# Kernel optimization log

Measured on AMD Instinct MI355X. Metric: run time of the kernel, lower is better.

The kernel has to match this reference:

```python
import jax, jax.numpy as jnp
import numpy as np

INPUTDIM = 256
OUTDIM = 64
GRIDSIZE = 300
BATCH = 2048


def setup_inputs() -> dict:
    key = jax.random.key(0)
    kx, kw = jax.random.split(key)
    x = jax.random.normal(kx, (BATCH, INPUTDIM), dtype=jnp.float32)
    stddev = 1.0 / (np.sqrt(INPUTDIM) * np.sqrt(GRIDSIZE))
    fouriercoeffs = jax.random.normal(kw, (2, OUTDIM, INPUTDIM, GRIDSIZE), dtype=jnp.float32) * stddev
    return {"x": x, "fouriercoeffs": fouriercoeffs}


def reference(x, fouriercoeffs):
    # k: frequencies 1..gridsize, shape [gridsize]
    gridsize = fouriercoeffs.shape[-1]
    k = jnp.arange(1, gridsize + 1, dtype=x.dtype)
    # phase [batch, inputdim, gridsize]
    phase = x[:, :, None] * k[None, None, :]
    c = jnp.cos(phase)
    s = jnp.sin(phase)
    # y[b,j] = sum_{i,k} c[b,i,k]*Wc[j,i,k] + s[b,i,k]*Ws[j,i,k]
    y = jnp.einsum('bik,jik->bj', c, fouriercoeffs[0]) + jnp.einsum('bik,jik->bj', s, fouriercoeffs[1])
    return y
```

## Files before the change

kernel.cpp:

```cpp
#include <hip/hip_runtime.h>
#include <hip/hip_bf16.h>

#define BATCH 2048
#define IDIM  256
#define ODIM  64
#define GRIDN 300

typedef __bf16 bf16x8 __attribute__((ext_vector_type(8)));
typedef float  f32x16 __attribute__((ext_vector_type(16)));
typedef float  f32x2  __attribute__((ext_vector_type(2)));
typedef unsigned int uint4v __attribute__((ext_vector_type(4)));

#define AS1 __attribute__((address_space(1)))
#define AS3 __attribute__((address_space(3)))

__device__ __forceinline__ unsigned short f2bf(float f) {
    return __builtin_bit_cast(unsigned short, __float2bfloat16(f));
}

__global__ __launch_bounds__(256) void fkan_prep(const float* __restrict__ fc,
                                                 char* __restrict__ wp) {
    __shared__ alignas(16) char lds[32768];
    const int blk = blockIdx.x;
    const int ib  = blk & 15;
    const int gb  = blk >> 4;
    const int g0  = gb * 8;
    const int G   = (gb == 37) ? 4 : 8;
    const int q   = threadIdx.x >> 6;
    const int j   = threadIdx.x & 63;

    float vals[2][4][8];
    #pragma unroll
    for (int t = 0; t < 2; ++t) {
        #pragma unroll
        for (int e = 0; e < 4; ++e) {
            const float* src = fc + (((size_t)t * ODIM + j) * IDIM
                                     + (ib * 16 + q * 4 + e)) * GRIDN + g0;
            float4 lo = *(const float4*)(src);
            vals[t][e][0] = lo.x; vals[t][e][1] = lo.y;
            vals[t][e][2] = lo.z; vals[t][e][3] = lo.w;
            if (G == 8) {
                float4 hi = *(const float4*)(src + 4);
                vals[t][e][4] = hi.x; vals[t][e][5] = hi.y;
                vals[t][e][6] = hi.z; vals[t][e][7] = hi.w;
            }
        }
    }
    #pragma unroll
    for (int g = 0; g < 8; ++g) {
        if (g < 4 || G == 8) {
            uint4v dw;
            #pragma unroll
            for (int e = 0; e < 4; ++e)
                dw[e] = (unsigned)f2bf(vals[0][e][g]) | ((unsigned)f2bf(vals[1][e][g]) << 16);
            *(uint4v*)(lds + g * 4096 + q * 1024 + j * 16) = dw;
        }
    }
    __syncthreads();
    char* dst = wp + ((size_t)ib * GRIDN + g0) * 4096;
    for (int w = threadIdx.x * 16; w < G * 4096; w += 256 * 16)
        *(uint4v*)(dst + w) = *(const uint4v*)(lds + w);
}

__global__ __launch_bounds__(256, 4) void fkan_main(const float* __restrict__ x,
                                                    const char* __restrict__ wp,
                                                    float* __restrict__ out) {
    __shared__ alignas(16) char lds[2][12288];

    const int bid    = blockIdx.x;
    const int xcd    = bid & 7;
    const int within = bid >> 3;
    const int slice  = xcd * 8 + (within & 7);
    const int mtile  = within >> 3;
    const int isplit = slice >> 2;
    const int gq     = slice & 3;
    const int g_begin = gq * 75;

    const int tid  = threadIdx.x;
    const int wave = tid >> 6;
    const int lane = tid & 63;
    const int l31  = lane & 31;
    const int kgrp = lane >> 5;
    const int row  = mtile * 128 + wave * 32 + l31;

    f32x2 vc[4], vs[4], vbc[4], vbs[4];
    const float* xrow = x + (size_t)row * IDIM + isplit * 16;
    #pragma unroll
    for (int h = 0; h < 2; ++h) {
        const float4 xv4 = *(const float4*)(xrow + h * 8 + kgrp * 4);
        float xa[4] = {xv4.x, xv4.y, xv4.z, xv4.w};
        #pragma unroll
        for (int p = 0; p < 4; ++p) {
            const int ss = h * 4 + p;
            const float xv = xa[p];
            float sb, cb;
            __sincosf(xv, &sb, &cb);
            vbc[ss >> 1][ss & 1] = cb; vbs[ss >> 1][ss & 1] = sb;
            float s0 = sb, c0 = cb;
            if (g_begin != 0) __sincosf((float)(g_begin + 1) * xv, &s0, &c0);
            vc[ss >> 1][ss & 1] = c0; vs[ss >> 1][ss & 1] = s0;
        }
    }

    const unsigned aq = (unsigned)kgrp * 1024 + (unsigned)l31 * 16;
    const char* wbase = wp + ((size_t)(isplit * GRIDN + g_begin)) * 4096 + tid * 16;

    #pragma unroll
    for (int p = 0; p < 3; ++p)
        __builtin_amdgcn_global_load_lds(
            (const AS1 unsigned int*)(wbase + (size_t)p * 4096),
            (AS3 unsigned int*)(&lds[0][0] + p * 4096 + tid * 16), 16, 0, 0);
    __syncthreads();

    f32x16 acc0 = {0,0,0,0,0,0,0,0,0,0,0,0,0,0,0,0};
    f32x16 acc1 = {0,0,0,0,0,0,0,0,0,0,0,0,0,0,0,0};

    for (int it = 0; it < 25; ++it) {
        const int cur = it & 1;
        if (it + 1 < 25) {
            #pragma unroll
            for (int p = 0; p < 3; ++p)
                __builtin_amdgcn_global_load_lds(
                    (const AS1 unsigned int*)(wbase + ((size_t)(it + 1) * 3 + p) * 4096),
                    (AS3 unsigned int*)(&lds[cur ^ 1][0] + p * 4096 + tid * 16),
                    16, 0, 0);
        }
        #pragma unroll
        for (int g = 0; g < 3; ++g) {
            const char* base = &lds[cur][0] + g * 4096;
            const bf16x8 b00 = *(const bf16x8*)(base + aq);
            const bf16x8 b01 = *(const bf16x8*)(base + aq + 512);
            const bf16x8 b10 = *(const bf16x8*)(base + aq + 2048);
            const bf16x8 b11 = *(const bf16x8*)(base + aq + 2560);
            uint4v a1, a2;
            #pragma unroll
            for (int p = 0; p < 4; ++p) {
                const float c1f = vc[p >> 1][p & 1],     s1f = vs[p >> 1][p & 1];
                const float c2f = vc[2 + (p >> 1)][p & 1], s2f = vs[2 + (p >> 1)][p & 1];
                unsigned r1, r2;
                asm("v_cvt_pk_bf16_f32 %0, %1, %2" : "=v"(r1) : "v"(c1f), "v"(s1f));
                asm("v_cvt_pk_bf16_f32 %0, %1, %2" : "=v"(r2) : "v"(c2f), "v"(s2f));
                a1[p] = r1; a2[p] = r2;
            }
            const bf16x8 af1 = __builtin_bit_cast(bf16x8, a1);
            const bf16x8 af2 = __builtin_bit_cast(bf16x8, a2);
            __builtin_amdgcn_s_setprio(1);
            acc0 = __builtin_amdgcn_mfma_f32_32x32x16_bf16(af1, b00, acc0, 0, 0, 0);
            acc1 = __builtin_amdgcn_mfma_f32_32x32x16_bf16(af1, b01, acc1, 0, 0, 0);
            acc0 = __builtin_amdgcn_mfma_f32_32x32x16_bf16(af2, b10, acc0, 0, 0, 0);
            acc1 = __builtin_amdgcn_mfma_f32_32x32x16_bf16(af2, b11, acc1, 0, 0, 0);
            __builtin_amdgcn_s_setprio(0);
            #pragma unroll
            for (int qq = 0; qq < 4; ++qq) {
                const f32x2 c = vc[qq], s = vs[qq];
                vc[qq] = c * vbc[qq] - s * vbs[qq];
                vs[qq] = s * vbc[qq] + c * vbs[qq];
            }
        }
        __syncthreads();
    }

    #pragma unroll
    for (int r = 0; r < 16; ++r) {
        const int orow = mtile * 128 + wave * 32 + (r & 3) + 8 * (r >> 2) + 4 * kgrp;
        unsafeAtomicAdd(out + (size_t)orow * ODIM + l31, acc0[r]);
        unsafeAtomicAdd(out + (size_t)orow * ODIM + 32 + l31, acc1[r]);
    }
}

__global__ __launch_bounds__(256) void fkan_naive(const float* __restrict__ x,
                                                  const float* __restrict__ fc,
                                                  float* __restrict__ out) {
    const int j = blockIdx.x >> 3;
    const int b = (blockIdx.x & 7) * 256 + threadIdx.x;
    const float* xr = x + (size_t)b * IDIM;
    float acc = 0.f;
    for (int i = 0; i < IDIM; ++i) {
        const float xv = xr[i];
        float sb, cb;
        __sincosf(xv, &sb, &cb);
        float c = cb, s = sb;
        const float* wc = fc + ((size_t)j * IDIM + i) * GRIDN;
        const float* ws = wc + (size_t)ODIM * IDIM * GRIDN;
        for (int g = 0; g < GRIDN; ++g) {
            acc += c * wc[g] + s * ws[g];
            const float cn = c * cb - s * sb;
            s = s * cb + c * sb;
            c = cn;
        }
    }
    out[(size_t)b * ODIM + j] = acc;
}

extern "C" void kernel_launch(void* const* d_in, const int* in_sizes, int n_in,
                              void* d_out, int out_size, void* d_ws, size_t ws_size,
                              hipStream_t stream) {
    const float* x  = (const float*)d_in[0];
    const float* fc = (const float*)d_in[1];
    float* out = (float*)d_out;
    constexpr size_t WPB = 16ull * GRIDN * 4096;

    if (ws_size >= WPB) {
        hipMemsetAsync(d_out, 0, (size_t)out_size * sizeof(float), stream);
        fkan_prep<<<608, 256, 0, stream>>>(fc, (char*)d_ws);
        fkan_main<<<1024, 256, 0, stream>>>(x, (const char*)d_ws, out);
    } else {
        fkan_naive<<<512, 256, 0, stream>>>(x, fc, out);
    }
}
```

Baseline: 78.58 us.

## Load weight fragments directly from global into registers, drop LDS staging

```diff
diff --git a/kernel.cpp b/kernel.cpp
--- a/kernel.cpp
+++ b/kernel.cpp
@@ -10,9 +10,6 @@
 typedef float  f32x16 __attribute__((ext_vector_type(16)));
 typedef float  f32x2  __attribute__((ext_vector_type(2)));
 typedef unsigned int uint4v __attribute__((ext_vector_type(4)));
-
-#define AS1 __attribute__((address_space(1)))
-#define AS3 __attribute__((address_space(3)))
 
 __device__ __forceinline__ unsigned short f2bf(float f) {
     return __builtin_bit_cast(unsigned short, __float2bfloat16(f));
@@ -65,8 +62,6 @@
 __global__ __launch_bounds__(256, 4) void fkan_main(const float* __restrict__ x,
                                                     const char* __restrict__ wp,
                                                     float* __restrict__ out) {
-    __shared__ alignas(16) char lds[2][12288];
-
     const int bid    = blockIdx.x;
     const int xcd    = bid & 7;
     const int within = bid >> 3;
@@ -83,7 +78,7 @@
     const int kgrp = lane >> 5;
     const int row  = mtile * 128 + wave * 32 + l31;
 
-    f32x2 vc[4], vs[4], vbc[4], vbs[4];
+    f32x2 vc[4], vs[4], vbc[4], vbs[4], vnbs[4];
     const float* xrow = x + (size_t)row * IDIM + isplit * 16;
     #pragma unroll
     for (int h = 0; h < 2; ++h) {
@@ -96,6 +91,7 @@
             float sb, cb;
             __sincosf(xv, &sb, &cb);
             vbc[ss >> 1][ss & 1] = cb; vbs[ss >> 1][ss & 1] = sb;
+            vnbs[ss >> 1][ss & 1] = -sb;
             float s0 = sb, c0 = cb;
             if (g_begin != 0) __sincosf((float)(g_begin + 1) * xv, &s0, &c0);
             vc[ss >> 1][ss & 1] = c0; vs[ss >> 1][ss & 1] = s0;
@@ -103,61 +99,53 @@
     }
 
     const unsigned aq = (unsigned)kgrp * 1024 + (unsigned)l31 * 16;
-    const char* wbase = wp + ((size_t)(isplit * GRIDN + g_begin)) * 4096 + tid * 16;
+    const char* curp = wp + ((size_t)(isplit * GRIDN + g_begin)) * 4096 + aq;
 
-    #pragma unroll
-    for (int p = 0; p < 3; ++p)
-        __builtin_amdgcn_global_load_lds(
-            (const AS1 unsigned int*)(wbase + (size_t)p * 4096),
-            (AS3 unsigned int*)(&lds[0][0] + p * 4096 + tid * 16), 16, 0, 0);
-    __syncthreads();
+    bf16x8 c0 = *(const bf16x8*)(curp);
+    bf16x8 c1 = *(const bf16x8*)(curp + 512);
+    bf16x8 c2 = *(const bf16x8*)(curp + 2048);
+    bf16x8 c3 = *(const bf16x8*)(curp + 2560);
 
     f32x16 acc0 = {0,0,0,0,0,0,0,0,0,0,0,0,0,0,0,0};
     f32x16 acc1 = {0,0,0,0,0,0,0,0,0,0,0,0,0,0,0,0};
 
-    for (int it = 0; it < 25; ++it) {
-        const int cur = it & 1;
-        if (it + 1 < 25) {
-            #pragma unroll
-            for (int p = 0; p < 3; ++p)
-                __builtin_amdgcn_global_load_lds(
-                    (const AS1 unsigned int*)(wbase + ((size_t)(it + 1) * 3 + p) * 4096),
-                    (AS3 unsigned int*)(&lds[cur ^ 1][0] + p * 4096 + tid * 16),
-                    16, 0, 0);
+    #pragma unroll 2
+    for (int it = 0; it < 75; ++it) {
+        const char* np = curp + (it < 74 ? 4096 : 0);
+        const bf16x8 n0 = *(const bf16x8*)(np);
+        const bf16x8 n1 = *(const bf16x8*)(np + 512);
+        const bf16x8 n2 = *(const bf16x8*)(np + 2048);
+        const bf16x8 n3 = *(const bf16x8*)(np + 2560);
+
+        uint4v a1, a2;
+        #pragma unroll
+        for (int p = 0; p < 4; ++p) {
+            const float c1f = vc[p >> 1][p & 1],       s1f = vs[p >> 1][p & 1];
+            const float c2f = vc[2 + (p >> 1)][p & 1], s2f = vs[2 + (p >> 1)][p & 1];
+            unsigned r1, r2;
+            asm("v_cvt_pk_bf16_f32 %0, %1, %2" : "=v"(r1) : "v"(c1f), "v"(s1f));
+            asm("v_cvt_pk_bf16_f32 %0, %1, %2" : "=v"(r2) : "v"(c2f), "v"(s2f));
+            a1[p] = r1; a2[p] = r2;
         }
+        const bf16x8 af1 = __builtin_bit_cast(bf16x8, a1);
+        const bf16x8 af2 = __builtin_bit_cast(bf16x8, a2);
+        __builtin_amdgcn_s_setprio(1);
+        acc0 = __builtin_amdgcn_mfma_f32_32x32x16_bf16(af1, c0, acc0, 0, 0, 0);
+        acc1 = __builtin_amdgcn_mfma_f32_32x32x16_bf16(af1, c1, acc1, 0, 0, 0);
+        acc0 = __builtin_amdgcn_mfma_f32_32x32x16_bf16(af2, c2, acc0, 0, 0, 0);
+        acc1 = __builtin_amdgcn_mfma_f32_32x32x16_bf16(af2, c3, acc1, 0, 0, 0);
+        __builtin_amdgcn_s_setprio(0);
         #pragma unroll
-        for (int g = 0; g < 3; ++g) {
-            const char* base = &lds[cur][0] + g * 4096;
-            const bf16x8 b00 = *(const bf16x8*)(base + aq);
-            const bf16x8 b01 = *(const bf16x8*)(base + aq + 512);
-            const bf16x8 b10 = *(const bf16x8*)(base + aq + 2048);
-            const bf16x8 b11 = *(const bf16x8*)(base + aq + 2560);
-            uint4v a1, a2;
-            #pragma unroll
-            for (int p = 0; p < 4; ++p) {
-                const float c1f = vc[p >> 1][p & 1],     s1f = vs[p >> 1][p & 1];
-                const float c2f = vc[2 + (p >> 1)][p & 1], s2f = vs[2 + (p >> 1)][p & 1];
-                unsigned r1, r2;
-                asm("v_cvt_pk_bf16_f32 %0, %1, %2" : "=v"(r1) : "v"(c1f), "v"(s1f));
-                asm("v_cvt_pk_bf16_f32 %0, %1, %2" : "=v"(r2) : "v"(c2f), "v"(s2f));
-                a1[p] = r1; a2[p] = r2;
-            }
-            const bf16x8 af1 = __builtin_bit_cast(bf16x8, a1);
-            const bf16x8 af2 = __builtin_bit_cast(bf16x8, a2);
-            __builtin_amdgcn_s_setprio(1);
-            acc0 = __builtin_amdgcn_mfma_f32_32x32x16_bf16(af1, b00, acc0, 0, 0, 0);
-            acc1 = __builtin_amdgcn_mfma_f32_32x32x16_bf16(af1, b01, acc1, 0, 0, 0);
-            acc0 = __builtin_amdgcn_mfma_f32_32x32x16_bf16(af2, b10, acc0, 0, 0, 0);
-            acc1 = __builtin_amdgcn_mfma_f32_32x32x16_bf16(af2, b11, acc1, 0, 0, 0);
-            __builtin_amdgcn_s_setprio(0);
-            #pragma unroll
-            for (int qq = 0; qq < 4; ++qq) {
-                const f32x2 c = vc[qq], s = vs[qq];
-                vc[qq] = c * vbc[qq] - s * vbs[qq];
-                vs[qq] = s * vbc[qq] + c * vbs[qq];
-            }
+        for (int qq = 0; qq < 4; ++qq) {
+            f32x2 t, u, cn, sn;
+            asm("v_pk_mul_f32 %0, %1, %2" : "=v"(t) : "v"(vs[qq]), "v"(vnbs[qq]));
+            asm("v_pk_mul_f32 %0, %1, %2" : "=v"(u) : "v"(vc[qq]), "v"(vbs[qq]));
+            asm("v_pk_fma_f32 %0, %1, %2, %3" : "=v"(cn) : "v"(vc[qq]), "v"(vbc[qq]), "v"(t));
+            asm("v_pk_fma_f32 %0, %1, %2, %3" : "=v"(sn) : "v"(vs[qq]), "v"(vbc[qq]), "v"(u));
+            vc[qq] = cn; vs[qq] = sn;
         }
-        __syncthreads();
+        c0 = n0; c1 = n1; c2 = n2; c3 = n3;
+        curp = np;
     }
 
     #pragma unroll
```

Result: slower. 86.17 us (+9.7%).
